# Kernel tuning notes

Hardware: AMD Instinct MI355X
Metric: run time of the kernel (lower is better)

## Reference

```python
import jax, jax.numpy as jnp
import numpy as np

E = 8            # num_experts
H = 1024         # hidden_size
I = 1024         # moe_intermediate_dim
T = 8192         # total tokens (sum of per-expert counts; no padding, grouped_mm path)
# Imbalanced routing, sums exactly to T
COUNTS = np.array([512, 1536, 1024, 768, 1280, 896, 1152, 1024], dtype=np.int32)


def setup_inputs() -> dict:
    key = jax.random.key(0)
    k_x, k_gu, k_d = jax.random.split(key, 3)
    x = jax.random.normal(k_x, (T, H), dtype=jnp.float32)
    # Weights stored pre-transposed: (E, H, 2I) and (E, I, H)
    gate_up_proj = jax.random.normal(k_gu, (E, H, 2 * I), dtype=jnp.float32) * (1.0 / np.sqrt(H))
    down_proj = jax.random.normal(k_d, (E, I, H), dtype=jnp.float32) * (1.0 / np.sqrt(I))
    num_tokens_per_expert = jnp.asarray(COUNTS)  # int32, sums to T
    return {
        "x": x,
        "gate_up_proj": gate_up_proj,
        "down_proj": down_proj,
        "num_tokens_per_expert": num_tokens_per_expert,
    }


def reference(x, gate_up_proj, down_proj, num_tokens_per_expert):
    # Grouped GEMM 1: [T,H] x [E,H,2I] with ragged group sizes -> [T,2I]
    gate_up = jax.lax.ragged_dot(x, gate_up_proj, group_sizes=num_tokens_per_expert)
    gate, up = jnp.split(gate_up, 2, axis=-1)
    h = jax.nn.silu(gate) * up  # SwiGLU: silu(gate) * up, [T,I]
    # Grouped GEMM 2: [T,I] x [E,I,H] -> [T,H]
    out = jax.lax.ragged_dot(h, down_proj, group_sizes=num_tokens_per_expert)
    return out.astype(x.dtype)
```

## Files before the change

### kernel.cpp

```cpp
#include <hip/hip_runtime.h>
#include <hip/hip_bf16.h>
#include <stdint.h>

#define E_ 8
#define H_ 1024
#define I_ 1024
#define T_ 8192
#define BM 128
#define BK 32
#define NKT 32

typedef __attribute__((ext_vector_type(4))) float f32x4;
typedef __attribute__((ext_vector_type(8))) short bf16x8;

__device__ __forceinline__ unsigned short f2bf(float f) {
  union { float f; unsigned int u; } v; v.f = f;
  unsigned int lsb = (v.u >> 16) & 1u;
  v.u += 0x7fffu + lsb;
  return (unsigned short)(v.u >> 16);
}

__device__ __forceinline__ void gload_lds16(const void* g, void* l) {
  __builtin_amdgcn_global_load_lds(
      (const __attribute__((address_space(1))) unsigned int*)g,
      (__attribute__((address_space(3))) unsigned int*)l,
      16, 0, 0);
}

__device__ __forceinline__ void find_tile(const int* counts, int ty,
                                          int& row_start, int& rows, int& expert) {
  int tacc = 0, off = 0;
  expert = 0; row_start = 0; rows = BM;
  #pragma unroll
  for (int e = 0; e < E_; ++e) {
    int c = counts[e];
    int te = (c + BM - 1) >> 7;
    if (ty >= tacc && ty < tacc + te) {
      expert = e;
      int lt = ty - tacc;
      row_start = off + lt * BM;
      rows = min(BM, c - lt * BM);
    }
    tacc += te; off += c;
  }
}

__device__ __forceinline__ void transpose_role(const float* inp,
                                               unsigned short* outp,
                                               int R, int C, int bx, int by,
                                               void* smem) {
  float (*tile)[33] = reinterpret_cast<float(*)[33]>(smem);
  int c0 = bx * 32, r0 = by * 64;
  int tx = threadIdx.x & 31, ty = threadIdx.x >> 5;
  for (int rr = ty; rr < 64; rr += 8)
    tile[rr][tx] = inp[(size_t)(r0 + rr) * C + c0 + tx];
  __syncthreads();
  for (int cc = ty; cc < 32; cc += 8) {
    ushort2 o;
    o.x = f2bf(tile[2 * tx][cc]);
    o.y = f2bf(tile[2 * tx + 1][cc]);
    *reinterpret_cast<ushort2*>(&outp[(size_t)(c0 + cc) * R + r0 + 2 * tx]) = o;
  }
}

__global__ __launch_bounds__(256) void preproc_union(
    const float* __restrict__ x, unsigned short* __restrict__ xb,
    const float* __restrict__ w1, unsigned short* __restrict__ w1t) {
  __shared__ float tile[64][33];
  int id = blockIdx.x;
  if (id < 8192) {
    int i = (id * 256 + threadIdx.x) * 4;
    float4 v = *reinterpret_cast<const float4*>(x + i);
    ushort4 o;
    o.x = f2bf(v.x); o.y = f2bf(v.y); o.z = f2bf(v.z); o.w = f2bf(v.w);
    *reinterpret_cast<ushort4*>(xb + i) = o;
    return;
  }
  int tb = id - 8192;
  int bx = tb & 63, by = (tb >> 6) & 15, bz = tb >> 10;
  transpose_role(w1 + (size_t)bz * H_ * 2 * I_,
                 w1t + (size_t)bz * H_ * 2 * I_, H_, 2 * I_, bx, by, tile);
}

#define G1LDS (BM * BK + 256 * BK)
__global__ __launch_bounds__(256, 2) void gemm1_union(
    const unsigned short* __restrict__ X,
    const unsigned short* __restrict__ W1T,
    const int* __restrict__ counts,
    unsigned short* __restrict__ Hout,
    const float* __restrict__ w2, unsigned short* __restrict__ w2t) {
  __shared__ unsigned short pool[3 * G1LDS];
  if (blockIdx.x < 4096) {
    int tb = blockIdx.x;
    int bx = tb & 31, by = (tb >> 5) & 15, bz = tb >> 9;
    transpose_role(w2 + (size_t)bz * I_ * H_,
                   w2t + (size_t)bz * I_ * H_, I_, H_, bx, by, pool);
    return;
  }
  int id = blockIdx.x - 4096;
  int swz = (id & 7) * 64 + (id >> 3);
  int bn = swz & 7;
  int tyid = swz >> 3;
  int row_start, rows, expert;
  find_tile(counts, tyid, row_start, rows, expert);
  int tid = threadIdx.x, wid = tid >> 6, lane = tid & 63;
  const unsigned short* Wp = W1T + (size_t)expert * (2 * I_) * H_;

  f32x4 acc[8][4];
  #pragma unroll
  for (int m = 0; m < 8; ++m)
    #pragma unroll
    for (int n = 0; n < 4; ++n) acc[m][n] = {0.f, 0.f, 0.f, 0.f};

  int l4 = lane >> 2;
  int csw = ((lane & 3) ^ ((l4 >> 1) & 3)) * 8;
  int lr = lane & 15;
  int ck = ((lane >> 4) ^ ((lr >> 1) & 3)) * 8;

#define STAGE1(buf, kt) do {                                                   \
    int k0 = (kt) * BK + csw;                                                  \
    unsigned short* Ab = pool + (buf) * G1LDS;                                 \
    unsigned short* Bb = Ab + BM * BK;                                         \
    _Pragma("unroll")                                                          \
    for (int i = 0; i < 2; ++i) {                                              \
      int r = wid * 32 + i * 16;                                               \
      int gr = row_start + min(r + l4, rows - 1);                              \
      gload_lds16(X + (size_t)gr * H_ + k0, Ab + r * BK);                      \
    }                                                                          \
    _Pragma("unroll")                                                          \
    for (int i = 0; i < 4; ++i) {                                              \
      int r = wid * 64 + i * 16;                                               \
      int rb = r + l4;                                                         \
      int sub = rb & 63, ow = rb >> 6;                                         \
      int col = (sub < 32) ? (bn * 128 + ow * 32 + sub)                        \
                           : (I_ + bn * 128 + ow * 32 + sub - 32);             \
      gload_lds16(Wp + (size_t)col * H_ + k0, Bb + r * BK);                    \
    }                                                                          \
  } while (0)

  STAGE1(0, 0);
  STAGE1(1, 1);
  for (int kt = 0; kt < NKT; ++kt) {
    STAGE1((kt + 2) % 3, min(kt + 2, NKT - 1));
    asm volatile("s_waitcnt vmcnt(12)" ::: "memory");
    __builtin_amdgcn_sched_barrier(0);
    __builtin_amdgcn_s_barrier();
    const unsigned short* Ab = pool + (kt % 3) * G1LDS;
    const unsigned short* Bb = Ab + BM * BK;
    bf16x8 a[8], b[4];
    #pragma unroll
    for (int m = 0; m < 8; ++m)
      a[m] = *reinterpret_cast<const bf16x8*>(&Ab[(m * 16 + lr) * BK + ck]);
    #pragma unroll
    for (int n = 0; n < 4; ++n)
      b[n] = *reinterpret_cast<const bf16x8*>(&Bb[(wid * 64 + n * 16 + lr) * BK + ck]);
    __builtin_amdgcn_s_setprio(1);
    #pragma unroll
    for (int m = 0; m < 8; ++m)
      #pragma unroll
      for (int n = 0; n < 4; ++n)
        acc[m][n] = __builtin_amdgcn_mfma_f32_16x16x32_bf16(a[m], b[n], acc[m][n], 0, 0, 0);
    __builtin_amdgcn_s_setprio(0);
    __builtin_amdgcn_sched_barrier(0);
    __builtin_amdgcn_s_barrier();
  }
#undef STAGE1

  int lq = lane >> 4;
  #pragma unroll
  for (int m = 0; m < 8; ++m)
    #pragma unroll
    for (int n = 0; n < 2; ++n) {
      f32x4 g = acc[m][n], u = acc[m][n + 2];
      #pragma unroll
      for (int r = 0; r < 4; ++r) {
        int rl = m * 16 + lq * 4 + r;
        if (rl < rows) {
          float gv = g[r];
          float hv = (gv / (1.f + __expf(-gv))) * u[r];
          Hout[(size_t)(row_start + rl) * I_ + bn * 128 + wid * 32 + n * 16 + lr] = f2bf(hv);
        }
      }
    }
}

#define G2LDS (BM * BK + BM * BK)
__global__ __launch_bounds__(256, 3) void gemm2(
    const unsigned short* __restrict__ Hin,
    const unsigned short* __restrict__ W2T,
    const int* __restrict__ counts,
    float* __restrict__ Out) {
  __shared__ unsigned short pool[3 * G2LDS];
  int id = blockIdx.x;
  int swz = (id & 7) * 64 + (id >> 3);
  int bn = swz & 7;
  int tyid = swz >> 3;
  int row_start, rows, expert;
  find_tile(counts, tyid, row_start, rows, expert);
  int tid = threadIdx.x, wid = tid >> 6, lane = tid & 63;
  int wr = wid >> 1, wc = wid & 1;
  const unsigned short* Wp = W2T + (size_t)expert * H_ * I_;

  f32x4 acc[4][4];
  #pragma unroll
  for (int m = 0; m < 4; ++m)
    #pragma unroll
    for (int n = 0; n < 4; ++n) acc[m][n] = {0.f, 0.f, 0.f, 0.f};

  int l4 = lane >> 2;
  int csw = ((lane & 3) ^ ((l4 >> 1) & 3)) * 8;
  int lr = lane & 15;
  int ck = ((lane >> 4) ^ ((lr >> 1) & 3)) * 8;

#define STAGE2(buf, kt) do {                                                   \
    int k0 = (kt) * BK + csw;                                                  \
    unsigned short* Ab = pool + (buf) * G2LDS;                                 \
    unsigned short* Bb = Ab + BM * BK;                                         \
    _Pragma("unroll")                                                          \
    for (int i = 0; i < 2; ++i) {                                              \
      int r = wid * 32 + i * 16;                                               \
      int gr = row_start + min(r + l4, rows - 1);                              \
      gload_lds16(Hin + (size_t)gr * I_ + k0, Ab + r * BK);                    \
    }                                                                          \
    _Pragma("unroll")                                                          \
    for (int i = 0; i < 2; ++i) {                                              \
      int r = wid * 32 + i * 16;                                               \
      int col = bn * 128 + r + l4;                                             \
      gload_lds16(Wp + (size_t)col * I_ + k0, Bb + r * BK);                    \
    }                                                                          \
  } while (0)

  STAGE2(0, 0);
  STAGE2(1, 1);
  for (int kt = 0; kt < NKT; ++kt) {
    STAGE2((kt + 2) % 3, min(kt + 2, NKT - 1));
    asm volatile("s_waitcnt vmcnt(8)" ::: "memory");
    __builtin_amdgcn_sched_barrier(0);
    __builtin_amdgcn_s_barrier();
    const unsigned short* Ab = pool + (kt % 3) * G2LDS;
    const unsigned short* Bb = Ab + BM * BK;
    bf16x8 a[4], b[4];
    #pragma unroll
    for (int m = 0; m < 4; ++m)
      a[m] = *reinterpret_cast<const bf16x8*>(&Ab[(wr * 64 + m * 16 + lr) * BK + ck]);
    #pragma unroll
    for (int n = 0; n < 4; ++n)
      b[n] = *reinterpret_cast<const bf16x8*>(&Bb[(wc * 64 + n * 16 + lr) * BK + ck]);
    __builtin_amdgcn_s_setprio(1);
    #pragma unroll
    for (int m = 0; m < 4; ++m)
      #pragma unroll
      for (int n = 0; n < 4; ++n)
        acc[m][n] = __builtin_amdgcn_mfma_f32_16x16x32_bf16(a[m], b[n], acc[m][n], 0, 0, 0);
    __builtin_amdgcn_s_setprio(0);
    __builtin_amdgcn_sched_barrier(0);
    __builtin_amdgcn_s_barrier();
  }
#undef STAGE2

  int lq = lane >> 4;
  #pragma unroll
  for (int m = 0; m < 4; ++m)
    #pragma unroll
    for (int n = 0; n < 4; ++n)
      #pragma unroll
      for (int r = 0; r < 4; ++r) {
        int rl = wr * 64 + m * 16 + lq * 4 + r;
        if (rl < rows)
          Out[(size_t)(row_start + rl) * H_ + bn * 128 + wc * 64 + n * 16 + lr] =
              acc[m][n][r];
      }
}

extern "C" void kernel_launch(void* const* d_in, const int* in_sizes, int n_in,
                              void* d_out, int out_size, void* d_ws, size_t ws_size,
                              hipStream_t stream) {
  const float* x  = (const float*)d_in[0];
  const float* w1 = (const float*)d_in[1];
  const float* w2 = (const float*)d_in[2];
  const int* counts = (const int*)d_in[3];
  float* out = (float*)d_out;

  char* ws = (char*)d_ws;
  unsigned short* xb  = (unsigned short*)ws;
  unsigned short* w1t = (unsigned short*)(ws + (size_t)T_ * H_ * 2);
  unsigned short* w2t = (unsigned short*)(ws + (size_t)T_ * H_ * 2
                                             + (size_t)E_ * 2 * I_ * H_ * 2);
  unsigned short* hbuf = (unsigned short*)(ws + (size_t)T_ * H_ * 2
                                              + (size_t)E_ * 2 * I_ * H_ * 2
                                              + (size_t)E_ * H_ * I_ * 2);

  preproc_union<<<16384, 256, 0, stream>>>(x, xb, w1, w1t);
  gemm1_union<<<4096 + 512, 256, 0, stream>>>(xb, w1t, counts, hbuf, w2, w2t);
  gemm2<<<512, 256, 0, stream>>>(hbuf, w2t, counts, out);
}
```

Before: 109.0 us.

## Widen gemm2 tile to 128x256 and schedule GEMM blocks before transposes

gemm2 moves from a 128x128 tile with a 2x2 warp layout to a 128x256 tile where each warp covers all 128 rows and 64 columns, matching gemm1. This halves the grid to 256 blocks and raises reuse of each loaded A tile, at the cost of more accumulator registers and lower occupancy (launch bounds drop from 3 to 2). In gemm1_union, the 512 GEMM blocks now get the low block indices and the w2 transpose blocks follow, so the GEMM work is dispatched first. The trailing sched_barrier in both main loops is also removed.

```diff
diff --git a/kernel.cpp b/kernel.cpp
--- a/kernel.cpp
+++ b/kernel.cpp
@@ -82,22 +82,22 @@
                  w1t + (size_t)bz * H_ * 2 * I_, H_, 2 * I_, bx, by, tile);
 }
 
-#define G1LDS (BM * BK + 256 * BK)
+#define GLDS (BM * BK + 256 * BK)
 __global__ __launch_bounds__(256, 2) void gemm1_union(
     const unsigned short* __restrict__ X,
     const unsigned short* __restrict__ W1T,
     const int* __restrict__ counts,
     unsigned short* __restrict__ Hout,
     const float* __restrict__ w2, unsigned short* __restrict__ w2t) {
-  __shared__ unsigned short pool[3 * G1LDS];
-  if (blockIdx.x < 4096) {
-    int tb = blockIdx.x;
+  __shared__ unsigned short pool[3 * GLDS];
+  if (blockIdx.x >= 512) {
+    int tb = blockIdx.x - 512;
     int bx = tb & 31, by = (tb >> 5) & 15, bz = tb >> 9;
     transpose_role(w2 + (size_t)bz * I_ * H_,
                    w2t + (size_t)bz * I_ * H_, I_, H_, bx, by, pool);
     return;
   }
-  int id = blockIdx.x - 4096;
+  int id = blockIdx.x;
   int swz = (id & 7) * 64 + (id >> 3);
   int bn = swz & 7;
   int tyid = swz >> 3;
@@ -119,7 +119,7 @@
 
 #define STAGE1(buf, kt) do {                                                   \
     int k0 = (kt) * BK + csw;                                                  \
-    unsigned short* Ab = pool + (buf) * G1LDS;                                 \
+    unsigned short* Ab = pool + (buf) * GLDS;                                  \
     unsigned short* Bb = Ab + BM * BK;                                         \
     _Pragma("unroll")                                                          \
     for (int i = 0; i < 2; ++i) {                                              \
@@ -145,7 +145,7 @@
     asm volatile("s_waitcnt vmcnt(12)" ::: "memory");
     __builtin_amdgcn_sched_barrier(0);
     __builtin_amdgcn_s_barrier();
-    const unsigned short* Ab = pool + (kt % 3) * G1LDS;
+    const unsigned short* Ab = pool + (kt % 3) * GLDS;
     const unsigned short* Bb = Ab + BM * BK;
     bf16x8 a[8], b[4];
     #pragma unroll
@@ -161,7 +161,6 @@
       for (int n = 0; n < 4; ++n)
         acc[m][n] = __builtin_amdgcn_mfma_f32_16x16x32_bf16(a[m], b[n], acc[m][n], 0, 0, 0);
     __builtin_amdgcn_s_setprio(0);
-    __builtin_amdgcn_sched_barrier(0);
     __builtin_amdgcn_s_barrier();
   }
 #undef STAGE1
@@ -184,26 +183,24 @@
     }
 }
 
-#define G2LDS (BM * BK + BM * BK)
-__global__ __launch_bounds__(256, 3) void gemm2(
+__global__ __launch_bounds__(256, 2) void gemm2(
     const unsigned short* __restrict__ Hin,
     const unsigned short* __restrict__ W2T,
     const int* __restrict__ counts,
     float* __restrict__ Out) {
-  __shared__ unsigned short pool[3 * G2LDS];
+  __shared__ unsigned short pool[3 * GLDS];
   int id = blockIdx.x;
-  int swz = (id & 7) * 64 + (id >> 3);
-  int bn = swz & 7;
-  int tyid = swz >> 3;
+  int swz = (id & 7) * 32 + (id >> 3);
+  int bn = swz & 3;
+  int tyid = swz >> 2;
   int row_start, rows, expert;
   find_tile(counts, tyid, row_start, rows, expert);
   int tid = threadIdx.x, wid = tid >> 6, lane = tid & 63;
-  int wr = wid >> 1, wc = wid & 1;
   const unsigned short* Wp = W2T + (size_t)expert * H_ * I_;
 
-  f32x4 acc[4][4];
-  #pragma unroll
-  for (int m = 0; m < 4; ++m)
+  f32x4 acc[8][4];
+  #pragma unroll
+  for (int m = 0; m < 8; ++m)
     #pragma unroll
     for (int n = 0; n < 4; ++n) acc[m][n] = {0.f, 0.f, 0.f, 0.f};
 
@@ -214,7 +211,7 @@
 
 #define STAGE2(buf, kt) do {                                                   \
     int k0 = (kt) * BK + csw;                                                  \
-    unsigned short* Ab = pool + (buf) * G2LDS;                                 \
+    unsigned short* Ab = pool + (buf) * GLDS;                                  \
     unsigned short* Bb = Ab + BM * BK;                                         \
     _Pragma("unroll")                                                          \
     for (int i = 0; i < 2; ++i) {                                              \
@@ -223,9 +220,9 @@
       gload_lds16(Hin + (size_t)gr * I_ + k0, Ab + r * BK);                    \
     }                                                                          \
     _Pragma("unroll")                                                          \
-    for (int i = 0; i < 2; ++i) {                                              \
-      int r = wid * 32 + i * 16;                                               \
-      int col = bn * 128 + r + l4;                                             \
+    for (int i = 0; i < 4; ++i) {                                              \
+      int r = wid * 64 + i * 16;                                               \
+      int col = bn * 256 + r + l4;                                             \
       gload_lds16(Wp + (size_t)col * I_ + k0, Bb + r * BK);                    \
     }                                                                          \
   } while (0)
@@ -234,40 +231,39 @@
   STAGE2(1, 1);
   for (int kt = 0; kt < NKT; ++kt) {
     STAGE2((kt + 2) % 3, min(kt + 2, NKT - 1));
-    asm volatile("s_waitcnt vmcnt(8)" ::: "memory");
+    asm volatile("s_waitcnt vmcnt(12)" ::: "memory");
     __builtin_amdgcn_sched_barrier(0);
     __builtin_amdgcn_s_barrier();
-    const unsigned short* Ab = pool + (kt % 3) * G2LDS;
+    const unsigned short* Ab = pool + (kt % 3) * GLDS;
     const unsigned short* Bb = Ab + BM * BK;
-    bf16x8 a[4], b[4];
-    #pragma unroll
-    for (int m = 0; m < 4; ++m)
-      a[m] = *reinterpret_cast<const bf16x8*>(&Ab[(wr * 64 + m * 16 + lr) * BK + ck]);
+    bf16x8 a[8], b[4];
+    #pragma unroll
+    for (int m = 0; m < 8; ++m)
+      a[m] = *reinterpret_cast<const bf16x8*>(&Ab[(m * 16 + lr) * BK + ck]);
     #pragma unroll
     for (int n = 0; n < 4; ++n)
-      b[n] = *reinterpret_cast<const bf16x8*>(&Bb[(wc * 64 + n * 16 + lr) * BK + ck]);
+      b[n] = *reinterpret_cast<const bf16x8*>(&Bb[(wid * 64 + n * 16 + lr) * BK + ck]);
     __builtin_amdgcn_s_setprio(1);
     #pragma unroll
-    for (int m = 0; m < 4; ++m)
+    for (int m = 0; m < 8; ++m)
       #pragma unroll
       for (int n = 0; n < 4; ++n)
         acc[m][n] = __builtin_amdgcn_mfma_f32_16x16x32_bf16(a[m], b[n], acc[m][n], 0, 0, 0);
     __builtin_amdgcn_s_setprio(0);
-    __builtin_amdgcn_sched_barrier(0);
     __builtin_amdgcn_s_barrier();
   }
 #undef STAGE2
 
   int lq = lane >> 4;
   #pragma unroll
-  for (int m = 0; m < 4; ++m)
+  for (int m = 0; m < 8; ++m)
     #pragma unroll
     for (int n = 0; n < 4; ++n)
       #pragma unroll
       for (int r = 0; r < 4; ++r) {
-        int rl = wr * 64 + m * 16 + lq * 4 + r;
+        int rl = m * 16 + lq * 4 + r;
         if (rl < rows)
-          Out[(size_t)(row_start + rl) * H_ + bn * 128 + wc * 64 + n * 16 + lr] =
+          Out[(size_t)(row_start + rl) * H_ + bn * 256 + wid * 64 + n * 16 + lr] =
               acc[m][n][r];
       }
 }
@@ -291,6 +287,6 @@
                                               + (size_t)E_ * H_ * I_ * 2);
 
   preproc_union<<<16384, 256, 0, stream>>>(x, xb, w1, w1t);
-  gemm1_union<<<4096 + 512, 256, 0, stream>>>(xb, w1t, counts, hbuf, w2, w2t);
-  gemm2<<<512, 256, 0, stream>>>(hbuf, w2t, counts, out);
-}
+  gemm1_union<<<512 + 4096, 256, 0, stream>>>(xb, w1t, counts, hbuf, w2, w2t);
+  gemm2<<<256, 256, 0, stream>>>(hbuf, w2t, counts, out);
+}
```

After: 108.1 us. About the same (-0.8%).
